# Kernel tuning notes

Hardware: AMD Instinct MI355X
Metric: run time of the kernel (lower is better)

The kernel has to match this reference:

```python
import jax, jax.numpy as jnp
import numpy as np

EPS = 1e-7
PI = np.pi


def _vel_to_R(vel):
    # vel: [..., 3] -> rotation matrix [..., 3, 3] (ZY convention from spherical angles)
    rho = jnp.linalg.norm(vel, axis=-1, keepdims=True)
    theta = jnp.arctan2(vel[..., 1:2], vel[..., 0:1])
    theta = theta + (theta < 0).astype(theta.dtype) * (2.0 * PI)  # symmetric_theta=False
    phi = jnp.arccos(jnp.clip(vel[..., 2:3] / (rho + EPS), -1.0, 1.0))
    ct, st = jnp.cos(theta)[..., 0], jnp.sin(theta)[..., 0]
    cp, sp = jnp.cos(phi)[..., 0], jnp.sin(phi)[..., 0]
    z = jnp.zeros_like(ct)
    R = jnp.stack([
        jnp.stack([cp * ct, -st, sp * ct], -1),
        jnp.stack([cp * st, ct, sp * st], -1),
        jnp.stack([-sp, z, cp], -1),
    ], -2)
    return R


def _rotate(R, x):
    return jnp.einsum('...ij,...j->...i', R, x)


def setup_inputs() -> dict:
    key = jax.random.key(0)
    B, N, H, D = 128, 100, 128, 3
    in_size = 2 * D  # 6
    nef = 3 * D + D * (D - 1) // 2 + in_size  # 18 edge features
    ks = jax.random.split(key, 12)

    inputs = jax.random.normal(ks[0], (B, N, in_size), jnp.float32)

    # fully connected edges (no self loops)
    send_np, recv_np = np.nonzero(~np.eye(N, dtype=bool))
    send_edges = jnp.asarray(send_np, jnp.int32)
    recv_edges = jnp.asarray(recv_np, jnp.int32)

    def lin(k, fin, fout):
        return jax.random.normal(k, (fin, fout), jnp.float32) / np.sqrt(fin)

    return dict(
        inputs=inputs,
        W1=lin(ks[1], nef, H), b1=jnp.zeros((H,), jnp.float32),
        W2=lin(ks[2], H, H), b2=jnp.zeros((H,), jnp.float32),
        Wr=lin(ks[3], in_size, H), br=jnp.zeros((H,), jnp.float32),
        W3=lin(ks[4], H, H), b3=jnp.zeros((H,), jnp.float32),
        W4=lin(ks[5], H, H), b4=jnp.zeros((H,), jnp.float32),
        W5=lin(ks[6], H, in_size), b5=jnp.zeros((in_size,), jnp.float32),
        send_edges=send_edges, recv_edges=recv_edges,
    )


def reference(inputs, W1, b1, W2, b2, Wr, br, W3, b3, W4, b4, W5, b5,
              send_edges, recv_edges):
    D = 3
    B, N, _ = inputs.shape

    # ---- Localizer.canonicalize_inputs ----
    vel = inputs[..., D:2 * D]
    Rnode = _vel_to_R(vel)                       # [B,N,3,3]
    Rinv_node = jnp.swapaxes(Rnode, -1, -2)
    canon_vel = _rotate(Rinv_node, vel)
    rel_feat = jnp.concatenate([jnp.zeros_like(canon_vel), canon_vel], -1)  # [B,N,6]

    # ---- Localizer.create_edge_attr ----
    x_j = inputs[:, send_edges]                  # [B,E,6] senders
    x_i = inputs[:, recv_edges]                  # [B,E,6] receivers
    R = _vel_to_R(x_i[..., D:2 * D])
    R_inv = jnp.swapaxes(R, -1, -2)
    rel_pos = x_j[..., :D] - x_i[..., :D]
    rot_rel = _rotate(R_inv, rel_pos)
    send_R = _vel_to_R(x_j[..., D:2 * D])
    rot_or = R_inv @ send_R
    euler = jnp.stack([
        jnp.arctan2(rot_or[..., 1, 0], rot_or[..., 0, 0]),
        jnp.arcsin(-rot_or[..., 2, 0]),
        jnp.arctan2(rot_or[..., 2, 1], rot_or[..., 2, 2]),
    ], -1) / PI
    dist = jnp.linalg.norm(rel_pos, axis=-1, keepdims=True)
    rho_e = jnp.linalg.norm(rot_rel, axis=-1, keepdims=True)
    theta_e = jnp.arctan2(rot_rel[..., 1:2], rot_rel[..., 0:1])  # symmetric theta
    phi_e = jnp.arccos(jnp.clip(rot_rel[..., 2:3] / (rho_e + EPS), -1.0, 1.0))
    rot_vel = _rotate(R_inv, x_j[..., D:2 * D])
    edge_attr = jnp.concatenate(
        [rot_rel, euler, dist, theta_e, phi_e, rot_vel], -1)   # [B,E,12]
    edge_attr = jnp.concatenate([edge_attr, rel_feat[:, recv_edges]], -1)  # [B,E,18]

    # ---- GNN: edge MLP + scatter-mean + out MLP (dropout off in eval) ----
    h = jax.nn.silu(edge_attr @ W1 + b1) @ W2 + b2               # [B,E,H]
    agg = jnp.zeros((B, N, h.shape[-1]), h.dtype).at[:, recv_edges].add(h)
    cnt = jnp.zeros((N,), h.dtype).at[recv_edges].add(1.0)
    agg = agg / jnp.maximum(cnt, 1.0)[None, :, None]             # scatter mean
    aug = agg + rel_feat @ Wr + br
    p = jax.nn.relu(aug @ W3 + b3)
    p = jax.nn.relu(p @ W4 + b4)
    pred = p @ W5 + b5                                           # [B,N,6]

    # ---- Globalizer: rotate each 3-vector chunk back to global frame ----
    gl = jnp.concatenate(
        [_rotate(Rnode, pred[..., i:i + D]) for i in range(0, pred.shape[-1], D)], -1)
    return inputs + gl
```

## Files before the change

### kernel.cpp

```cpp
#include <hip/hip_runtime.h>
#include <math.h>

#define EPSF 1e-7f
constexpr int NN  = 100;
constexpr int DEG = 99;
constexpr int IN  = 6;
constexpr int H   = 128;
constexpr int G   = 4;
constexpr float INV_PI = 0.3183098861837907f;
constexpr float LOG2E  = 1.4426950408889634f;
constexpr float LN2    = 0.6931471805599453f;

typedef __attribute__((ext_vector_type(4))) _Float16 half4;
typedef __attribute__((ext_vector_type(8))) _Float16 half8;
typedef __attribute__((ext_vector_type(4))) float f32x4;

constexpr int XST = 144;
constexpr int SXS = 15;

__device__ __forceinline__ float clampf(float x, float lo, float hi) {
    return fminf(fmaxf(x, lo), hi);
}
__device__ __forceinline__ float sig2(float y) {
    return __builtin_amdgcn_rcpf(1.f + __builtin_amdgcn_exp2f(-y));
}
__device__ __forceinline__ float fast_atan2(float y, float x) {
    float ax = fabsf(x), ay = fabsf(y);
    float mx = fmaxf(ax, ay), mn = fminf(ax, ay);
    float r = mn * __builtin_amdgcn_rcpf(fmaxf(mx, 1e-35f));
    float r2 = r * r;
    float p = fmaf(r2, -0.0851330f, 0.1801410f);
    p = fmaf(r2, p, -0.3302995f);
    p = fmaf(r2, p, 0.9998660f);
    float t = r * p;
    t = (ay > ax) ? (1.5707963267948966f - t) : t;
    t = (x < 0.f) ? (3.14159265358979323f - t) : t;
    return copysignf(t, y);
}
__device__ __forceinline__ float fast_asin(float z) {
    return fast_atan2(z, sqrtf(fmaxf(0.f, (1.f - z) * (1.f + z))));
}
__device__ __forceinline__ float fast_acos(float z) {
    return fast_atan2(sqrtf(fmaxf(0.f, (1.f - z) * (1.f + z))), z);
}
__device__ __forceinline__ void vel_to_R(float vx, float vy, float vz, float* R) {
    float rho = sqrtf(vx * vx + vy * vy + vz * vz);
    float rxy = sqrtf(vx * vx + vy * vy);
    float inv = __builtin_amdgcn_rcpf(rxy);
    bool big = rxy > 1e-30f;
    float ct = big ? vx * inv : 1.f;
    float st = big ? vy * inv : 0.f;
    float cp = clampf(vz * __builtin_amdgcn_rcpf(rho + EPSF), -1.f, 1.f);
    float sp = sqrtf(fmaxf(0.f, 1.f - cp * cp));
    R[0] = cp * ct; R[1] = -st; R[2] = sp * ct;
    R[3] = cp * st; R[4] = ct;  R[5] = sp * st;
    R[6] = -sp;     R[7] = 0.f; R[8] = cp;
}

__global__ void conv_w(const float* __restrict__ W1, const float* __restrict__ W2,
                       const float* __restrict__ W3, const float* __restrict__ W4,
                       half4* __restrict__ w1f, half8* __restrict__ wmlp) {
    int t = blockIdx.x * blockDim.x + threadIdx.x;
    if (t >= 104 * 64) return;
    int L = t & 63, f = t >> 6;
    int m = L & 15, qd = L >> 4;
    if (f < 8) {
        int n = f * 16 + m;
        half4 v;
#pragma unroll
        for (int j = 0; j < 4; ++j) {
            int k = qd * 4 + j;
            v[j] = (k < 12) ? (_Float16)(W1[k * H + n] * LOG2E) : (_Float16)0.f;
        }
        w1f[f * 64 + L] = v;
    } else {
        int ff = f - 8;
        int layer = ff >> 5, rest = ff & 31;
        int kt = rest >> 3, nt = rest & 7;
        const float* W = (layer == 0) ? W2 : (layer == 1) ? W3 : W4;
        float scale = (layer == 0) ? LN2 : 1.f;
        int n = nt * 16 + m;
        half8 v;
#pragma unroll
        for (int j = 0; j < 8; ++j)
            v[j] = (_Float16)(W[(kt * 32 + qd * 8 + j) * H + n] * scale);
        wmlp[((layer * 4 + kt) * 8 + nt) * 64 + L] = v;
    }
}

__global__ __launch_bounds__(128)
void locs_fused(const float* __restrict__ in,
                const float* __restrict__ W1, const float* __restrict__ b1,
                const float* __restrict__ b2,
                const float* __restrict__ Wr, const float* __restrict__ br,
                const float* __restrict__ b3, const float* __restrict__ b4,
                const float* __restrict__ W5, const float* __restrict__ b5,
                const half4* __restrict__ w1f, const half8* __restrict__ wmlp,
                float* __restrict__ out) {
    __shared__ half4 eaA[2 * 7 * 64];
    __shared__ float sxr[NN * SXS];
    __shared__ float poolF[1056];
    __shared__ _Float16 xh[G * XST];

    float* baseF = poolF;
    float* xFp   = poolF + 512;
    float* cvF   = poolF + 1040;
    float* pbF   = poolF;
    float* predF = poolF + 384;

    const int tid = threadIdx.x;
    const int L   = tid & 63;
    const int wv  = tid >> 6;
    const int lm  = L & 15;
    const int bn0 = blockIdx.x * G;
    const int bB  = bn0 / NN;
    const int n0  = bn0 - bB * NN;

    {
        half4 z = {0, 0, 0, 0};
#pragma unroll
        for (int i = 0; i < 7; ++i) eaA[tid + i * 128] = z;
    }
    if (tid < NN) {
        const float* xi = in + (bB * NN + tid) * IN;
        float R[9];
        float px = xi[0], py = xi[1], pz = xi[2];
        float vx = xi[3], vy = xi[4], vz = xi[5];
        vel_to_R(vx, vy, vz, R);
        float* dst = sxr + tid * SXS;
#pragma unroll
        for (int k = 0; k < 9; ++k) dst[k] = R[k];
        dst[9] = px; dst[10] = py; dst[11] = pz;
        dst[12] = vx; dst[13] = vy; dst[14] = vz;
    }
    __syncthreads();
    if (tid < G) {
        const float* rg = sxr + (n0 + tid) * SXS;
        float vx = rg[12], vy = rg[13], vz = rg[14];
        cvF[tid * 4 + 0] = rg[0] * vx + rg[3] * vy + rg[6] * vz;
        cvF[tid * 4 + 1] = rg[1] * vx + rg[4] * vy + rg[7] * vz;
        cvF[tid * 4 + 2] = rg[2] * vx + rg[5] * vy + rg[8] * vz;
    }
    __syncthreads();

    {
        float w15 = W1[15 * H + tid], w16 = W1[16 * H + tid], w17 = W1[17 * H + tid];
        float b1c = b1[tid];
#pragma unroll
        for (int g = 0; g < G; ++g)
            baseF[g * 128 + tid] = (b1c + cvF[g * 4 + 0] * w15
                                  + cvF[g * 4 + 1] * w16 + cvF[g * 4 + 2] * w17) * LOG2E;
    }
    half4 bfr[4];
#pragma unroll
    for (int i = 0; i < 4; ++i) bfr[i] = w1f[(wv * 4 + i) * 64 + L];

    auto edge_features = [&](int g, int buf) {
        if (tid < DEG) {
            int nG = n0 + g;
            int s = tid < nG ? tid : tid + 1;
            const float* rn = sxr + nG * SXS;
            const float* rs = sxr + s * SXS;
            float Rn[9];
#pragma unroll
            for (int k = 0; k < 9; ++k) Rn[k] = rn[k];
            float rel0 = rs[9] - rn[9], rel1 = rs[10] - rn[10], rel2 = rs[11] - rn[11];
            float vjx = rs[12], vjy = rs[13], vjz = rs[14];
            float Rs0 = rs[0], Rs1 = rs[1], Rs2 = rs[2];
            float Rs3 = rs[3], Rs4 = rs[4], Rs5 = rs[5];
            float Rs6 = rs[6], Rs7 = rs[7], Rs8 = rs[8];
            float rr0 = Rn[0] * rel0 + Rn[3] * rel1 + Rn[6] * rel2;
            float rr1 = Rn[1] * rel0 + Rn[4] * rel1 + Rn[7] * rel2;
            float rr2 = Rn[2] * rel0 + Rn[5] * rel1 + Rn[8] * rel2;
            float ro00 = Rn[0] * Rs0 + Rn[3] * Rs3 + Rn[6] * Rs6;
            float ro10 = Rn[1] * Rs0 + Rn[4] * Rs3 + Rn[7] * Rs6;
            float ro20 = Rn[2] * Rs0 + Rn[5] * Rs3 + Rn[8] * Rs6;
            float ro21 = Rn[2] * Rs1 + Rn[5] * Rs4 + Rn[8] * Rs7;
            float ro22 = Rn[2] * Rs2 + Rn[5] * Rs5 + Rn[8] * Rs8;
            float dist = sqrtf(rel0 * rel0 + rel1 * rel1 + rel2 * rel2);
            half4 f0, f1, f2;
            f0[0] = (_Float16)rr0; f0[1] = (_Float16)rr1; f0[2] = (_Float16)rr2;
            f0[3] = (_Float16)(fast_atan2(ro10, ro00) * INV_PI);
            f1[0] = (_Float16)(fast_asin(clampf(-ro20, -1.f, 1.f)) * INV_PI);
            f1[1] = (_Float16)(fast_atan2(ro21, ro22) * INV_PI);
            f1[2] = (_Float16)dist;
            f1[3] = (_Float16)fast_atan2(rr1, rr0);
            f2[0] = (_Float16)fast_acos(clampf(rr2 * __builtin_amdgcn_rcpf(dist + EPSF), -1.f, 1.f));
            f2[1] = (_Float16)(Rn[0] * vjx + Rn[3] * vjy + Rn[6] * vjz);
            f2[2] = (_Float16)(Rn[1] * vjx + Rn[4] * vjy + Rn[7] * vjz);
            f2[3] = (_Float16)(Rn[2] * vjx + Rn[5] * vjy + Rn[8] * vjz);
            int t = tid >> 4, m = tid & 15;
            half4* dst = eaA + buf * 448 + t * 64;
            dst[m]      = f0;
            dst[16 + m] = f1;
            dst[32 + m] = f2;
        }
    };

    edge_features(0, 0);
    __syncthreads();

#pragma unroll
    for (int g = 0; g < G; ++g) {
        float part[4] = {0.f, 0.f, 0.f, 0.f};
        float bs[4];
        f32x4 c[4];
#pragma unroll
        for (int i = 0; i < 4; ++i) {
            bs[i] = baseF[g * 128 + wv * 64 + i * 16 + lm];
            c[i] = (f32x4){bs[i], bs[i], bs[i], bs[i]};
        }
        const half4* ea = eaA + (g & 1) * 448;
#pragma unroll
        for (int t = 0; t < 7; ++t) {
            half4 a = ea[t * 64 + L];
            f32x4 d0 = __builtin_amdgcn_mfma_f32_16x16x16f16(a, bfr[0], c[0], 0, 0, 0);
            f32x4 d1 = __builtin_amdgcn_mfma_f32_16x16x16f16(a, bfr[1], c[1], 0, 0, 0);
            f32x4 d2 = __builtin_amdgcn_mfma_f32_16x16x16f16(a, bfr[2], c[2], 0, 0, 0);
            f32x4 d3 = __builtin_amdgcn_mfma_f32_16x16x16f16(a, bfr[3], c[3], 0, 0, 0);
#pragma unroll
            for (int r = 0; r < 4; ++r) {
                part[0] += d0[r] * sig2(d0[r]);
                part[1] += d1[r] * sig2(d1[r]);
                part[2] += d2[r] * sig2(d2[r]);
                part[3] += d3[r] * sig2(d3[r]);
            }
        }
        if (g < G - 1) edge_features(g + 1, (g + 1) & 1);
#pragma unroll
        for (int i = 0; i < 4; ++i) {
            float v = part[i];
            v += __shfl_xor(v, 16, 64);
            v += __shfl_xor(v, 32, 64);
            if (L < 16)
                xFp[g * 132 + wv * 64 + i * 16 + L] = v - 13.f * bs[i] * sig2(bs[i]);
        }
        __syncthreads();
    }

    const int q = L >> 4;
#pragma unroll
    for (int layer = 0; layer < 3; ++layer) {
#pragma unroll
        for (int r = 0; r < G; ++r)
            xh[r * XST + tid] = (_Float16)xFp[r * 132 + tid];
        __syncthreads();
        int rowb = (lm & 3) * XST;
        half8 ah[4];
#pragma unroll
        for (int kt = 0; kt < 4; ++kt)
            ah[kt] = *(const half8*)&xh[rowb + kt * 32 + q * 8];
        f32x4 acc[4];
#pragma unroll
        for (int i = 0; i < 4; ++i) acc[i] = (f32x4){0.f, 0.f, 0.f, 0.f};
#pragma unroll
        for (int kt = 0; kt < 4; ++kt) {
            int base = ((layer * 4 + kt) * 8 + wv * 4) * 64 + L;
#pragma unroll
            for (int i = 0; i < 4; ++i) {
                half8 bh = wmlp[base + i * 64];
                acc[i] = __builtin_amdgcn_mfma_f32_16x16x32_f16(ah[kt], bh, acc[i], 0, 0, 0);
            }
        }
        __syncthreads();
        if (L < 16) {
#pragma unroll
            for (int i = 0; i < 4; ++i) {
                int ch = wv * 64 + i * 16 + lm;
                if (layer == 0) {
                    float b2c = b2[ch], brc = br[ch];
                    float w3c = Wr[3 * H + ch], w4c = Wr[4 * H + ch], w5c = Wr[5 * H + ch];
#pragma unroll
                    for (int r = 0; r < 4; ++r)
                        xFp[r * 132 + ch] = acc[i][r] * (1.f / 99.f) + b2c
                                          + cvF[r * 4 + 0] * w3c + cvF[r * 4 + 1] * w4c
                                          + cvF[r * 4 + 2] * w5c + brc;
                } else {
                    float bb = (layer == 1) ? b3[ch] : b4[ch];
#pragma unroll
                    for (int r = 0; r < 4; ++r)
                        xFp[r * 132 + ch] = fmaxf(0.f, acc[i][r] + bb);
                }
            }
        }
        __syncthreads();
    }

    if (tid < 96) {
        int o = tid >> 4, sl = tid & 15, kb = sl * 8;
        float w5[8];
#pragma unroll
        for (int j = 0; j < 8; ++j) w5[j] = W5[(kb + j) * IN + o];
#pragma unroll
        for (int g = 0; g < G; ++g) {
            float s = 0.f;
#pragma unroll
            for (int j = 0; j < 8; ++j) s = fmaf(xFp[g * 132 + kb + j], w5[j], s);
            pbF[g * 96 + sl * 6 + o] = s;
        }
    }
    __syncthreads();
    if (tid < 24) {
        int g = tid / 6, o = tid - g * 6;
        float s = b5[o];
#pragma unroll
        for (int sl = 0; sl < 16; ++sl) s += pbF[g * 96 + sl * 6 + o];
        predF[g * 8 + o] = s;
    }
    __syncthreads();
    if (tid < 24) {
        int g = tid / 6, o = tid - g * 6;
        int r = (o < 3) ? o : o - 3;
        int off = (o < 3) ? 0 : 3;
        const float* Rg = sxr + (n0 + g) * SXS;
        float gl = Rg[r * 3 + 0] * predF[g * 8 + off + 0]
                 + Rg[r * 3 + 1] * predF[g * 8 + off + 1]
                 + Rg[r * 3 + 2] * predF[g * 8 + off + 2];
        int bng = bn0 + g;
        out[bng * IN + o] = Rg[9 + o] + gl;
    }
}

extern "C" void kernel_launch(void* const* d_in, const int* in_sizes, int n_in,
                              void* d_out, int out_size, void* d_ws, size_t ws_size,
                              hipStream_t stream) {
    const float* in = (const float*)d_in[0];
    const float* W1 = (const float*)d_in[1];
    const float* b1 = (const float*)d_in[2];
    const float* W2 = (const float*)d_in[3];
    const float* b2 = (const float*)d_in[4];
    const float* Wr = (const float*)d_in[5];
    const float* br = (const float*)d_in[6];
    const float* W3 = (const float*)d_in[7];
    const float* b3 = (const float*)d_in[8];
    const float* W4 = (const float*)d_in[9];
    const float* b4 = (const float*)d_in[10];
    const float* W5 = (const float*)d_in[11];
    const float* b5 = (const float*)d_in[12];
    float* out = (float*)d_out;

    half4* w1f  = (half4*)d_ws;
    half8* wmlp = (half8*)((char*)d_ws + 4096);

    const int BN = in_sizes[0] / IN;
    conv_w<<<26, 256, 0, stream>>>(W1, W2, W3, W4, w1f, wmlp);
    locs_fused<<<BN / G, 128, 0, stream>>>(in, W1, b1, b2, Wr, br, b3, b4,
                                           W5, b5, w1f, wmlp, out);
}
```

Baseline: 157.8 us.

## Interleave edges of all four nodes in MFMA tiles to cut padding

Edge-feature tiles are re-laid out so each 16-row MFMA tile holds 4 edges from each of the 4 nodes in the block. That shrinks padding from 13 wasted rows per node to 1, and it lets each lane accumulate one node's rows directly without cross-lane shuffles. All 396 edge features are now built up front in one phase, replacing the double-buffered per-node loop. This removes three barriers and some MFMA and sigmoid work. The cost is that feature computation no longer overlaps with the matrix math, and the LDS buffer grows, with a stride of 65 to avoid bank conflicts.

```diff
diff --git a/kernel.cpp b/kernel.cpp
--- a/kernel.cpp
+++ b/kernel.cpp
@@ -17,6 +17,8 @@
 
 constexpr int XST = 144;
 constexpr int SXS = 15;
+constexpr int TS  = 65;
+constexpr int NT  = 25;
 
 __device__ __forceinline__ float clampf(float x, float lo, float hi) {
     return fminf(fmaxf(x, lo), hi);
@@ -97,7 +99,7 @@
                 const float* __restrict__ W5, const float* __restrict__ b5,
                 const half4* __restrict__ w1f, const half8* __restrict__ wmlp,
                 float* __restrict__ out) {
-    __shared__ half4 eaA[2 * 7 * 64];
+    __shared__ half4 eaA[NT * TS];
     __shared__ float sxr[NN * SXS];
     __shared__ float poolF[1056];
     __shared__ _Float16 xh[G * XST];
@@ -111,16 +113,13 @@
     const int tid = threadIdx.x;
     const int L   = tid & 63;
     const int wv  = tid >> 6;
+    const int q   = L >> 4;
     const int lm  = L & 15;
     const int bn0 = blockIdx.x * G;
     const int bB  = bn0 / NN;
     const int n0  = bn0 - bB * NN;
 
-    {
-        half4 z = {0, 0, 0, 0};
-#pragma unroll
-        for (int i = 0; i < 7; ++i) eaA[tid + i * 128] = z;
-    }
+    for (int i = tid; i < NT * TS; i += 128) eaA[i] = (half4){0, 0, 0, 0};
     if (tid < NN) {
         const float* xi = in + (bB * NN + tid) * IN;
         float R[9];
@@ -155,10 +154,14 @@
 #pragma unroll
     for (int i = 0; i < 4; ++i) bfr[i] = w1f[(wv * 4 + i) * 64 + L];
 
-    auto edge_features = [&](int g, int buf) {
-        if (tid < DEG) {
+#pragma unroll
+    for (int rnd = 0; rnd < 4; ++rnd) {
+        int j = tid + rnd * 128;
+        if (j < G * DEG) {
+            int g = j / DEG;
+            int e = j - g * DEG;
             int nG = n0 + g;
-            int s = tid < nG ? tid : tid + 1;
+            int s = e < nG ? e : e + 1;
             const float* rn = sxr + nG * SXS;
             const float* rs = sxr + s * SXS;
             float Rn[9];
@@ -189,31 +192,27 @@
             f2[1] = (_Float16)(Rn[0] * vjx + Rn[3] * vjy + Rn[6] * vjz);
             f2[2] = (_Float16)(Rn[1] * vjx + Rn[4] * vjy + Rn[7] * vjz);
             f2[3] = (_Float16)(Rn[2] * vjx + Rn[5] * vjy + Rn[8] * vjz);
-            int t = tid >> 4, m = tid & 15;
-            half4* dst = eaA + buf * 448 + t * 64;
-            dst[m]      = f0;
-            dst[16 + m] = f1;
-            dst[32 + m] = f2;
-        }
-    };
-
-    edge_features(0, 0);
-    __syncthreads();
-
-#pragma unroll
-    for (int g = 0; g < G; ++g) {
-        float part[4] = {0.f, 0.f, 0.f, 0.f};
-        float bs[4];
+            int t = e >> 2;
+            int mrow = g * 4 + (e & 3);
+            half4* dst = eaA + t * TS + mrow;
+            dst[0]  = f0;
+            dst[16] = f1;
+            dst[32] = f2;
+        }
+    }
+    __syncthreads();
+
+    {
+        float bs[4], part[4] = {0.f, 0.f, 0.f, 0.f};
         f32x4 c[4];
 #pragma unroll
         for (int i = 0; i < 4; ++i) {
-            bs[i] = baseF[g * 128 + wv * 64 + i * 16 + lm];
+            bs[i] = baseF[q * 128 + wv * 64 + i * 16 + lm];
             c[i] = (f32x4){bs[i], bs[i], bs[i], bs[i]};
         }
-        const half4* ea = eaA + (g & 1) * 448;
-#pragma unroll
-        for (int t = 0; t < 7; ++t) {
-            half4 a = ea[t * 64 + L];
+#pragma unroll
+        for (int t = 0; t < NT; ++t) {
+            half4 a = eaA[t * TS + L];
             f32x4 d0 = __builtin_amdgcn_mfma_f32_16x16x16f16(a, bfr[0], c[0], 0, 0, 0);
             f32x4 d1 = __builtin_amdgcn_mfma_f32_16x16x16f16(a, bfr[1], c[1], 0, 0, 0);
             f32x4 d2 = __builtin_amdgcn_mfma_f32_16x16x16f16(a, bfr[2], c[2], 0, 0, 0);
@@ -226,19 +225,14 @@
                 part[3] += d3[r] * sig2(d3[r]);
             }
         }
-        if (g < G - 1) edge_features(g + 1, (g + 1) & 1);
 #pragma unroll
         for (int i = 0; i < 4; ++i) {
-            float v = part[i];
-            v += __shfl_xor(v, 16, 64);
-            v += __shfl_xor(v, 32, 64);
-            if (L < 16)
-                xFp[g * 132 + wv * 64 + i * 16 + L] = v - 13.f * bs[i] * sig2(bs[i]);
-        }
-        __syncthreads();
-    }
-
-    const int q = L >> 4;
+            float v = part[i] - bs[i] * sig2(bs[i]);
+            xFp[q * 132 + wv * 64 + i * 16 + lm] = v;
+        }
+    }
+    __syncthreads();
+
 #pragma unroll
     for (int layer = 0; layer < 3; ++layer) {
 #pragma unroll
```

New measurement: 144.6 us. 1.09x faster.
